# Kernel tuning notes

Hardware: AMD Instinct MI355X
Metric: run time of the kernel (lower is better)

The kernel has to match this reference:

```python
import jax, jax.numpy as jnp
import numpy as np

N_STUDENT = 100000
N_COURSE = 20000
N_EDGES = 1000000
HIDDEN = 128


def setup_inputs() -> dict:
    key = jax.random.key(0)
    ks = jax.random.split(key, 8)
    scale = 1.0 / np.sqrt(2 * HIDDEN)
    return {
        "z_student": jax.random.normal(ks[0], (N_STUDENT, HIDDEN), dtype=jnp.float32),
        "z_course": jax.random.normal(ks[1], (N_COURSE, HIDDEN), dtype=jnp.float32),
        "row": jax.random.randint(ks[2], (N_EDGES,), 0, N_STUDENT, dtype=jnp.int64),
        "col": jax.random.randint(ks[3], (N_EDGES,), 0, N_COURSE, dtype=jnp.int64),
        "W1": jax.random.normal(ks[4], (2 * HIDDEN, HIDDEN), dtype=jnp.float32) * scale,
        "b1": jnp.zeros((HIDDEN,), dtype=jnp.float32),
        "W2": jax.random.normal(ks[5], (HIDDEN, 1), dtype=jnp.float32) * (1.0 / np.sqrt(HIDDEN)),
        "b2": jnp.zeros((1,), dtype=jnp.float32),
    }


def reference(z_student, z_course, row, col, W1, b1, W2, b2):
    # gather endpoint embeddings and concat along feature dim: [E, 2H]
    z = jnp.concatenate([z_student[row], z_course[col]], axis=-1)
    h = jax.nn.relu(z @ W1 + b1)   # [E, H]
    out = h @ W2 + b2              # [E, 1]
    return out.reshape(-1)
```

## Files before the change

### kernel.cpp

```cpp
#include <hip/hip_runtime.h>
#include <hip/hip_bf16.h>
#include <hip/hip_fp16.h>


typedef _Float16 half2v __attribute__((ext_vector_type(2)));
typedef _Float16 half8v __attribute__((ext_vector_type(8)));
typedef __fp16   fp16x2 __attribute__((ext_vector_type(2)));
typedef float    float4v __attribute__((ext_vector_type(4)));

#define NB   64
#define NR   8
#define CAPS 2176

__global__ __launch_bounds__(256) void conv_w(const float* __restrict__ W1,
                                              const float* __restrict__ W2,
                                              _Float16* __restrict__ Wt,
                                              _Float16* __restrict__ w2h,
                                              int* __restrict__ cnt) {
    int b = blockIdx.x, t = threadIdx.x;
    if (b == 8) {
        if (t < 128) w2h[t] = (_Float16)W2[t];
        for (int i = t; i < NB * NR; i += 256) cnt[i] = 0;
        return;
    }
    __shared__ _Float16 lds[32][136];
    int h = b >> 2, n0 = (b & 3) * 32;
    for (int i = 0; i < 16; ++i) {
        int idx = i * 256 + t;
        int k = idx >> 5, nn = idx & 31;
        lds[nn][k] = (_Float16)W1[(h * 128 + k) * 128 + n0 + nn];
    }
    __syncthreads();
    for (int j = 0; j < 2; ++j) {
        int idx = j * 256 + t;
        int nn = idx >> 4, kc = idx & 15;
        half8v v;
        #pragma unroll
        for (int q = 0; q < 8; ++q) v[q] = lds[nn][kc * 8 + q];
        *(half8v*)&Wt[((h * 128 + n0 + nn) * 128) + kc * 8] = v;
    }
}

__global__ __launch_bounds__(256) void gemm_u(
    const float* __restrict__ Zs, const float* __restrict__ Zc,
    const _Float16* __restrict__ Wt, const float* __restrict__ b1,
    _Float16* __restrict__ Us, _Float16* __restrict__ Uc,
    int Ms, int Mc, int nbs)
{
    __shared__ uint4 ldsW[2048];
    const int bid = blockIdx.x, t = threadIdx.x;

    const float* Z; _Float16* U; const _Float16* W; int M, m0, addB;
    if (bid < nbs) { Z = Zs; U = Us; M = Ms; m0 = bid * 64;         W = Wt;         addB = 1; }
    else           { Z = Zc; U = Uc; M = Mc; m0 = (bid - nbs) * 64; W = Wt + 16384; addB = 0; }

    const uint4* Wv = (const uint4*)W;
    #pragma unroll
    for (int i = 0; i < 8; ++i) {
        int j = i * 256 + t;
        int n = j >> 4, ch = j & 15;
        ldsW[n * 16 + (ch ^ ((n >> 3) & 7))] = Wv[j];
    }
    __syncthreads();

    const int wave = t >> 6, lane = t & 63, quad = lane >> 4, l16 = lane & 15;
    int mrow = m0 + wave * 16 + l16;
    int mload = mrow < M ? mrow : M - 1;
    const float* zrow = Z + (long)mload * 128;

    float4v acc[8];
    #pragma unroll
    for (int nt = 0; nt < 8; ++nt) acc[nt] = (float4v)(0.0f);

    #pragma unroll
    for (int c = 0; c < 4; ++c) {
        const float4v* pa = (const float4v*)(zrow + c * 32 + quad * 8);
        float4v a0 = pa[0], a1 = pa[1];
        fp16x2 p[4];
        p[0] = __builtin_amdgcn_cvt_pkrtz(a0[0], a0[1]);
        p[1] = __builtin_amdgcn_cvt_pkrtz(a0[2], a0[3]);
        p[2] = __builtin_amdgcn_cvt_pkrtz(a1[0], a1[1]);
        p[3] = __builtin_amdgcn_cvt_pkrtz(a1[2], a1[3]);
        half8v af;
        __builtin_memcpy(&af, &p[0], 16);
        const int ch = c * 4 + quad;
        #pragma unroll
        for (int nt = 0; nt < 8; ++nt) {
            const int n = l16 * 8 + nt;
            const half8v* pb = (const half8v*)&ldsW[n * 16 + (ch ^ (l16 & 7))];
            acc[nt] = __builtin_amdgcn_mfma_f32_16x16x32_f16(af, *pb, acc[nt], 0, 0, 0);
        }
    }

    float bv[8];
    if (addB) {
        const float4v* pb1 = (const float4v*)(b1 + l16 * 8);
        float4v x0 = pb1[0], x1 = pb1[1];
        bv[0]=x0[0]; bv[1]=x0[1]; bv[2]=x0[2]; bv[3]=x0[3];
        bv[4]=x1[0]; bv[5]=x1[1]; bv[6]=x1[2]; bv[7]=x1[3];
    } else {
        #pragma unroll
        for (int i = 0; i < 8; ++i) bv[i] = 0.0f;
    }

    const int rbase = m0 + wave * 16 + quad * 4;
    #pragma unroll
    for (int r = 0; r < 4; ++r) {
        int rr = rbase + r;
        if (rr < M) {
            half8v o;
            #pragma unroll
            for (int nt = 0; nt < 8; ++nt) o[nt] = (_Float16)(acc[nt][r] + bv[nt]);
            *(half8v*)&U[(long)rr * 128 + l16 * 8] = o;
        }
    }
}

__global__ __launch_bounds__(256) void bucket_scatter(
    const int* __restrict__ row, const int* __restrict__ col,
    long* __restrict__ rcB, int* __restrict__ pos,
    int* __restrict__ cnt, int E, float scale)
{
    __shared__ int hist[NB], base[NB], hist2[NB];
    const int t = threadIdx.x;
    const int rep = blockIdx.x & (NR - 1);
    if (t < NB) { hist[t] = 0; hist2[t] = 0; }
    __syncthreads();
    const long e0 = (long)blockIdx.x * 1024 + t;
    int r[4], c[4], bk[4];
    bool v[4];
    #pragma unroll
    for (int k = 0; k < 4; ++k) {
        long e = e0 + k * 256;
        v[k] = e < (long)E;
        long ee = v[k] ? e : 0;
        r[k] = __builtin_nontemporal_load(&row[ee]);
        c[k] = __builtin_nontemporal_load(&col[ee]);
        int b = (int)((float)r[k] * scale);
        bk[k] = b > NB - 1 ? NB - 1 : b;
        if (v[k]) atomicAdd(&hist[bk[k]], 1);
    }
    __syncthreads();
    if (t < NB) base[t] = atomicAdd(&cnt[t * NR + rep], hist[t]);
    __syncthreads();
    #pragma unroll
    for (int k = 0; k < 4; ++k) {
        if (!v[k]) continue;
        int o = atomicAdd(&hist2[bk[k]], 1);
        int slot = base[bk[k]] + o;
        long e = e0 + k * 256;
        int p = -1;
        if (slot < CAPS) {
            int g = (bk[k] * NR + rep) * CAPS + slot;
            long packed = ((long)(unsigned)r[k]) | (((long)(unsigned)c[k]) << 32);
            __builtin_nontemporal_store(packed, &rcB[g]);
            p = g;
        }
        __builtin_nontemporal_store(p, &pos[e]);
    }
}

__global__ __launch_bounds__(256) void edge_bucket(
    const long* __restrict__ rcB, const int* __restrict__ cnt,
    const _Float16* __restrict__ us, const _Float16* __restrict__ uc,
    const _Float16* __restrict__ w2h, const float* __restrict__ b2,
    float* __restrict__ outB)
{
    const int t = threadIdx.x, sub = t & 7;
    const int x = blockIdx.x & 7;
    const int l = blockIdx.x >> 3;
    const int p = l & 7;
    const int w = l >> 3;

    const uint4* pw = (const uint4*)(w2h + sub * 16);
    uint4 w0 = pw[0], w1 = pw[1];
    half2v W[8];
    *(uint4*)&W[0] = w0; *(uint4*)&W[4] = w1;
    const float bb = b2[0];
    const half2v zero = {(_Float16)0, (_Float16)0};

    #pragma unroll 1
    for (int bl = 0; bl < NB / 8; ++bl) {
        const int b = x * (NB / 8) + bl;
        const int ss = b * NR + p;
        int n = cnt[ss]; n = n < CAPS ? n : CAPS;
        const int seg = ss * CAPS;
        #pragma unroll 1
        for (int i0 = w * 32; i0 < n; i0 += 32 * 32) {
            int i = i0 + (t >> 3);
            bool act = i < n;
            int ii = act ? i : 0;
            long rc = __builtin_nontemporal_load(&rcB[seg + ii]);
            int r = (int)(rc & 0xffffffffL);
            int c = (int)(rc >> 32);
            const uint4* pa = (const uint4*)(us + (long)r * 128 + sub * 16);
            const uint4* pb = (const uint4*)(uc + (long)c * 128 + sub * 16);
            uint4 a0 = pa[0], a1 = pa[1];
            uint4 c0 = pb[0], c1 = pb[1];
            half2v A[8], B[8];
            *(uint4*)&A[0] = a0; *(uint4*)&A[4] = a1;
            *(uint4*)&B[0] = c0; *(uint4*)&B[4] = c1;
            float s = 0.0f;
            #pragma unroll
            for (int q = 0; q < 8; ++q) {
                half2v h = A[q] + B[q];
                h = __builtin_elementwise_max(h, zero);
                s += (float)h[0] * (float)W[q][0];
                s += (float)h[1] * (float)W[q][1];
            }
            s += __shfl_xor(s, 1);
            s += __shfl_xor(s, 2);
            s += __shfl_xor(s, 4);
            if (sub == 0 && act) outB[seg + i] = s + bb;
        }
    }
}

__global__ __launch_bounds__(256) void unscatter(
    const int* __restrict__ pos, const float* __restrict__ outB,
    const int* __restrict__ row, const int* __restrict__ col,
    const _Float16* __restrict__ us, const _Float16* __restrict__ uc,
    const _Float16* __restrict__ w2h, const float* __restrict__ b2,
    float* __restrict__ out, int E)
{
    const int t = threadIdx.x;
    #pragma unroll
    for (int k = 0; k < 4; ++k) {
        long e = (long)blockIdx.x * 1024 + k * 256 + t;
        if (e >= (long)E) return;
        int p = __builtin_nontemporal_load(&pos[e]);
        float s;
        if (p >= 0) {
            s = outB[p];
        } else {
            int r = row[e], c = col[e];
            s = b2[0];
            for (int kk = 0; kk < 128; ++kk) {
                float h = (float)us[(long)r * 128 + kk] + (float)uc[(long)c * 128 + kk];
                s += fmaxf(h, 0.0f) * (float)w2h[kk];
            }
        }
        __builtin_nontemporal_store(s, &out[e]);
    }
}

__global__ __launch_bounds__(256) void edge_kernel(
    const int* __restrict__ row, const int* __restrict__ col,
    const _Float16* __restrict__ us, const _Float16* __restrict__ uc,
    const _Float16* __restrict__ w2h, const float* __restrict__ b2,
    float* __restrict__ out, int E)
{
    const int t = threadIdx.x;
    const int sub = t & 7;
    long e = (long)blockIdx.x * 32 + (t >> 3);
    if (e >= E) return;
    int r = row[e], c = col[e];

    const uint4* pa = (const uint4*)(us  + (long)r * 128 + sub * 16);
    const uint4* pb = (const uint4*)(uc  + (long)c * 128 + sub * 16);
    const uint4* pw = (const uint4*)(w2h + sub * 16);
    uint4 a0 = pa[0], a1 = pa[1];
    uint4 c0 = pb[0], c1 = pb[1];
    uint4 w0 = pw[0], w1 = pw[1];

    half2v A[8], B[8], W[8];
    *(uint4*)&A[0] = a0; *(uint4*)&A[4] = a1;
    *(uint4*)&B[0] = c0; *(uint4*)&B[4] = c1;
    *(uint4*)&W[0] = w0; *(uint4*)&W[4] = w1;

    const half2v zero = {(_Float16)0, (_Float16)0};
    float s = 0.0f;
    #pragma unroll
    for (int i = 0; i < 8; ++i) {
        half2v h = A[i] + B[i];
        h = __builtin_elementwise_max(h, zero);
        s += (float)h[0] * (float)W[i][0];
        s += (float)h[1] * (float)W[i][1];
    }
    s += __shfl_xor(s, 1);
    s += __shfl_xor(s, 2);
    s += __shfl_xor(s, 4);
    if (sub == 0) out[e] = s + b2[0];
}

extern "C" void kernel_launch(void* const* d_in, const int* in_sizes, int n_in,
                              void* d_out, int out_size, void* d_ws, size_t ws_size,
                              hipStream_t stream) {
    const float* zs  = (const float*)d_in[0];
    const float* zc  = (const float*)d_in[1];
    const int*   row = (const int*)d_in[2];
    const int*   col = (const int*)d_in[3];
    const float* W1  = (const float*)d_in[4];
    const float* b1  = (const float*)d_in[5];
    const float* W2  = (const float*)d_in[6];
    const float* b2  = (const float*)d_in[7];
    float* out = (float*)d_out;

    const int Ms = in_sizes[0] / 128;
    const int Mc = in_sizes[1] / 128;
    const int E  = in_sizes[2];

    char* wsb = (char*)d_ws;
    _Float16* Wt  = (_Float16*)wsb;
    _Float16* w2h = (_Float16*)(wsb + 65536);
    int*      cnt = (int*)(wsb + 65792);
    size_t off = 67840;
    _Float16* us = (_Float16*)(wsb + off);  off += (size_t)Ms * 256;
    _Float16* uc = (_Float16*)(wsb + off);  off += (size_t)Mc * 256;
    long*  rcB  = (long*)(wsb + off);  off += (size_t)NB * NR * CAPS * 8;
    int*   pos  = (int*)(wsb + off);   off += (size_t)E * 4;
    float* outB = (float*)(wsb + off); off += (size_t)NB * NR * CAPS * 4;
    const bool bucketed = (off <= ws_size);

    const int nbs = (Ms + 63) / 64, nbc = (Mc + 63) / 64;

    conv_w<<<9, 256, 0, stream>>>(W1, W2, Wt, w2h, cnt);
    gemm_u<<<nbs + nbc, 256, 0, stream>>>(zs, zc, Wt, b1, us, uc, Ms, Mc, nbs);
    if (bucketed) {
        bucket_scatter<<<(E + 1023) / 1024, 256, 0, stream>>>(
            row, col, rcB, pos, cnt, E, (float)NB / (float)Ms);
        edge_bucket<<<2048, 256, 0, stream>>>(rcB, cnt, us, uc, w2h, b2, outB);
        unscatter<<<(E + 1023) / 1024, 256, 0, stream>>>(
            pos, outB, row, col, us, uc, w2h, b2, out, E);
    } else {
        edge_kernel<<<(E + 31) / 32, 256, 0, stream>>>(row, col, us, uc, w2h, b2, out, E);
    }
    (void)n_in; (void)out_size;
}
```

Before: 190.2 us.

## Fuse bucket scatter into GEMM launch, pack edge indices to 32 bits

The edge bucketing pass now runs as extra blocks of the projection GEMM kernel, so it overlaps with the GEMM and one launch is removed. Row and column indices are packed into a single 32-bit word (17 bits for row) instead of 64 bits, which halves the bucket buffer traffic. The bucket layout moves to 16 replicas with smaller capacity, and each edge-kernel thread now handles two edges per iteration for more memory-level parallelism. The 17-bit packing assumes fewer than 131072 students and fewer than 32768 courses, and the smaller per-bucket capacity makes overflow to the slow fallback path more likely.

```diff
diff --git a/kernel.cpp b/kernel.cpp
--- a/kernel.cpp
+++ b/kernel.cpp
@@ -9,8 +9,8 @@
 typedef float    float4v __attribute__((ext_vector_type(4)));
 
 #define NB   64
-#define NR   8
-#define CAPS 2176
+#define NR   16
+#define CAPS 1152
 
 __global__ __launch_bounds__(256) void conv_w(const float* __restrict__ W1,
                                               const float* __restrict__ W2,
@@ -41,15 +41,62 @@
     }
 }
 
-__global__ __launch_bounds__(256) void gemm_u(
+__global__ __launch_bounds__(256) void gemm_scatter(
     const float* __restrict__ Zs, const float* __restrict__ Zc,
     const _Float16* __restrict__ Wt, const float* __restrict__ b1,
     _Float16* __restrict__ Us, _Float16* __restrict__ Uc,
-    int Ms, int Mc, int nbs)
+    int Ms, int Mc, int nbs, int G,
+    const int* __restrict__ row, const int* __restrict__ col,
+    unsigned* __restrict__ rcB, int* __restrict__ pos,
+    int* __restrict__ cnt, int E, float scale)
 {
     __shared__ uint4 ldsW[2048];
-    const int bid = blockIdx.x, t = threadIdx.x;
-
+    const int t = threadIdx.x;
+
+    if ((int)blockIdx.x >= G) {
+        const int sb = blockIdx.x - G;
+        int* hist  = (int*)ldsW;
+        int* base  = hist + NB;
+        int* hist2 = hist + 2 * NB;
+        const int rep = sb & (NR - 1);
+        if (t < NB) { hist[t] = 0; hist2[t] = 0; }
+        __syncthreads();
+        const long e0 = (long)sb * 1024 + t;
+        int r[4], c[4], bk[4];
+        bool v[4];
+        #pragma unroll
+        for (int k = 0; k < 4; ++k) {
+            long e = e0 + k * 256;
+            v[k] = e < (long)E;
+            long ee = v[k] ? e : 0;
+            r[k] = __builtin_nontemporal_load(&row[ee]);
+            c[k] = __builtin_nontemporal_load(&col[ee]);
+            int b = (int)((float)r[k] * scale);
+            bk[k] = b > NB - 1 ? NB - 1 : b;
+            if (v[k]) atomicAdd(&hist[bk[k]], 1);
+        }
+        __syncthreads();
+        if (t < NB) base[t] = atomicAdd(&cnt[t * NR + rep], hist[t]);
+        __syncthreads();
+        #pragma unroll
+        for (int k = 0; k < 4; ++k) {
+            if (!v[k]) continue;
+            int o = atomicAdd(&hist2[bk[k]], 1);
+            int slot = base[bk[k]] + o;
+            long e = e0 + k * 256;
+            int p = -1;
+            if (slot < CAPS) {
+                int g = (bk[k] * NR + rep) * CAPS + slot;
+                unsigned packed = (unsigned)r[k] | ((unsigned)c[k] << 17);
+                __builtin_nontemporal_store(packed, &rcB[g]);
+                p = g;
+            }
+            __builtin_nontemporal_store(p, &pos[e]);
+        }
+        return;
+    }
+
+    const int bid = blockIdx.x;
     const float* Z; _Float16* U; const _Float16* W; int M, m0, addB;
     if (bid < nbs) { Z = Zs; U = Us; M = Ms; m0 = bid * 64;         W = Wt;         addB = 1; }
     else           { Z = Zc; U = Uc; M = Mc; m0 = (bid - nbs) * 64; W = Wt + 16384; addB = 0; }
@@ -116,61 +163,17 @@
     }
 }
 
-__global__ __launch_bounds__(256) void bucket_scatter(
-    const int* __restrict__ row, const int* __restrict__ col,
-    long* __restrict__ rcB, int* __restrict__ pos,
-    int* __restrict__ cnt, int E, float scale)
-{
-    __shared__ int hist[NB], base[NB], hist2[NB];
-    const int t = threadIdx.x;
-    const int rep = blockIdx.x & (NR - 1);
-    if (t < NB) { hist[t] = 0; hist2[t] = 0; }
-    __syncthreads();
-    const long e0 = (long)blockIdx.x * 1024 + t;
-    int r[4], c[4], bk[4];
-    bool v[4];
-    #pragma unroll
-    for (int k = 0; k < 4; ++k) {
-        long e = e0 + k * 256;
-        v[k] = e < (long)E;
-        long ee = v[k] ? e : 0;
-        r[k] = __builtin_nontemporal_load(&row[ee]);
-        c[k] = __builtin_nontemporal_load(&col[ee]);
-        int b = (int)((float)r[k] * scale);
-        bk[k] = b > NB - 1 ? NB - 1 : b;
-        if (v[k]) atomicAdd(&hist[bk[k]], 1);
-    }
-    __syncthreads();
-    if (t < NB) base[t] = atomicAdd(&cnt[t * NR + rep], hist[t]);
-    __syncthreads();
-    #pragma unroll
-    for (int k = 0; k < 4; ++k) {
-        if (!v[k]) continue;
-        int o = atomicAdd(&hist2[bk[k]], 1);
-        int slot = base[bk[k]] + o;
-        long e = e0 + k * 256;
-        int p = -1;
-        if (slot < CAPS) {
-            int g = (bk[k] * NR + rep) * CAPS + slot;
-            long packed = ((long)(unsigned)r[k]) | (((long)(unsigned)c[k]) << 32);
-            __builtin_nontemporal_store(packed, &rcB[g]);
-            p = g;
-        }
-        __builtin_nontemporal_store(p, &pos[e]);
-    }
-}
-
 __global__ __launch_bounds__(256) void edge_bucket(
-    const long* __restrict__ rcB, const int* __restrict__ cnt,
+    const unsigned* __restrict__ rcB, const int* __restrict__ cnt,
     const _Float16* __restrict__ us, const _Float16* __restrict__ uc,
     const _Float16* __restrict__ w2h, const float* __restrict__ b2,
     float* __restrict__ outB)
 {
-    const int t = threadIdx.x, sub = t & 7;
+    const int t = threadIdx.x, sub = t & 7, tg = t >> 3;
     const int x = blockIdx.x & 7;
     const int l = blockIdx.x >> 3;
-    const int p = l & 7;
-    const int w = l >> 3;
+    const int p = l & (NR - 1);
+    const int w = l >> 4;
 
     const uint4* pw = (const uint4*)(w2h + sub * 16);
     uint4 w0 = pw[0], w1 = pw[1];
@@ -186,32 +189,51 @@
         int n = cnt[ss]; n = n < CAPS ? n : CAPS;
         const int seg = ss * CAPS;
         #pragma unroll 1
-        for (int i0 = w * 32; i0 < n; i0 += 32 * 32) {
-            int i = i0 + (t >> 3);
-            bool act = i < n;
-            int ii = act ? i : 0;
-            long rc = __builtin_nontemporal_load(&rcB[seg + ii]);
-            int r = (int)(rc & 0xffffffffL);
-            int c = (int)(rc >> 32);
-            const uint4* pa = (const uint4*)(us + (long)r * 128 + sub * 16);
-            const uint4* pb = (const uint4*)(uc + (long)c * 128 + sub * 16);
-            uint4 a0 = pa[0], a1 = pa[1];
-            uint4 c0 = pb[0], c1 = pb[1];
-            half2v A[8], B[8];
-            *(uint4*)&A[0] = a0; *(uint4*)&A[4] = a1;
-            *(uint4*)&B[0] = c0; *(uint4*)&B[4] = c1;
-            float s = 0.0f;
+        for (int i0 = w * 64; i0 < n; i0 += 16 * 64) {
+            int i  = i0 + tg;
+            int i2 = i + 32;
+            bool a0v = i < n, a1v = i2 < n;
+            int ii  = a0v ? i  : 0;
+            int ii2 = a1v ? i2 : 0;
+            unsigned p0 = __builtin_nontemporal_load(&rcB[seg + ii]);
+            unsigned p1 = __builtin_nontemporal_load(&rcB[seg + ii2]);
+            int r0 = p0 & 0x1FFFF, c0 = p0 >> 17;
+            int r1 = p1 & 0x1FFFF, c1 = p1 >> 17;
+            const uint4* pa0 = (const uint4*)(us + (long)r0 * 128 + sub * 16);
+            const uint4* pb0 = (const uint4*)(uc + (long)c0 * 128 + sub * 16);
+            const uint4* pa1 = (const uint4*)(us + (long)r1 * 128 + sub * 16);
+            const uint4* pb1 = (const uint4*)(uc + (long)c1 * 128 + sub * 16);
+            uint4 a00 = pa0[0], a01 = pa0[1];
+            uint4 b00 = pb0[0], b01 = pb0[1];
+            uint4 a10 = pa1[0], a11 = pa1[1];
+            uint4 b10 = pb1[0], b11 = pb1[1];
+            half2v A0[8], B0[8], A1[8], B1[8];
+            *(uint4*)&A0[0] = a00; *(uint4*)&A0[4] = a01;
+            *(uint4*)&B0[0] = b00; *(uint4*)&B0[4] = b01;
+            *(uint4*)&A1[0] = a10; *(uint4*)&A1[4] = a11;
+            *(uint4*)&B1[0] = b10; *(uint4*)&B1[4] = b11;
+            float s0 = 0.0f, s1 = 0.0f;
             #pragma unroll
             for (int q = 0; q < 8; ++q) {
-                half2v h = A[q] + B[q];
-                h = __builtin_elementwise_max(h, zero);
-                s += (float)h[0] * (float)W[q][0];
-                s += (float)h[1] * (float)W[q][1];
+                half2v h0 = A0[q] + B0[q];
+                half2v h1 = A1[q] + B1[q];
+                h0 = __builtin_elementwise_max(h0, zero);
+                h1 = __builtin_elementwise_max(h1, zero);
+                s0 += (float)h0[0] * (float)W[q][0];
+                s0 += (float)h0[1] * (float)W[q][1];
+                s1 += (float)h1[0] * (float)W[q][0];
+                s1 += (float)h1[1] * (float)W[q][1];
             }
-            s += __shfl_xor(s, 1);
-            s += __shfl_xor(s, 2);
-            s += __shfl_xor(s, 4);
-            if (sub == 0 && act) outB[seg + i] = s + bb;
+            s0 += __shfl_xor(s0, 1);
+            s1 += __shfl_xor(s1, 1);
+            s0 += __shfl_xor(s0, 2);
+            s1 += __shfl_xor(s1, 2);
+            s0 += __shfl_xor(s0, 4);
+            s1 += __shfl_xor(s1, 4);
+            if (sub == 0) {
+                if (a0v) outB[seg + i]  = s0 + bb;
+                if (a1v) outB[seg + i2] = s1 + bb;
+            }
         }
     }
 }
@@ -304,21 +326,23 @@
     _Float16* Wt  = (_Float16*)wsb;
     _Float16* w2h = (_Float16*)(wsb + 65536);
     int*      cnt = (int*)(wsb + 65792);
-    size_t off = 67840;
+    size_t off = 69888;
     _Float16* us = (_Float16*)(wsb + off);  off += (size_t)Ms * 256;
     _Float16* uc = (_Float16*)(wsb + off);  off += (size_t)Mc * 256;
-    long*  rcB  = (long*)(wsb + off);  off += (size_t)NB * NR * CAPS * 8;
+    unsigned* rcB = (unsigned*)(wsb + off); off += (size_t)NB * NR * CAPS * 4;
     int*   pos  = (int*)(wsb + off);   off += (size_t)E * 4;
     float* outB = (float*)(wsb + off); off += (size_t)NB * NR * CAPS * 4;
     const bool bucketed = (off <= ws_size);
 
     const int nbs = (Ms + 63) / 64, nbc = (Mc + 63) / 64;
+    const int G = nbs + nbc;
+    const int SB = bucketed ? (E + 1023) / 1024 : 0;
 
     conv_w<<<9, 256, 0, stream>>>(W1, W2, Wt, w2h, cnt);
-    gemm_u<<<nbs + nbc, 256, 0, stream>>>(zs, zc, Wt, b1, us, uc, Ms, Mc, nbs);
+    gemm_scatter<<<G + SB, 256, 0, stream>>>(
+        zs, zc, Wt, b1, us, uc, Ms, Mc, nbs, G,
+        row, col, rcB, pos, cnt, E, (float)NB / (float)Ms);
     if (bucketed) {
-        bucket_scatter<<<(E + 1023) / 1024, 256, 0, stream>>>(
-            row, col, rcB, pos, cnt, E, (float)NB / (float)Ms);
         edge_bucket<<<2048, 256, 0, stream>>>(rcB, cnt, us, uc, w2h, b2, outB);
         unscatter<<<(E + 1023) / 1024, 256, 0, stream>>>(
             pos, outB, row, col, us, uc, w2h, b2, out, E);
```

Result: no change. 189.1 us (-0.6%).
